# Optimization experiments

Hardware: AMD Instinct MI355X
Metric: run time of the kernel (lower is better)

Reference implementation:

```python
import jax, jax.numpy as jnp
import numpy as np

B, N, D, H = 32, 64, 64, 4
E = 4 * D
HD = E // H
EPS = 1e-10
TAU = 1.0


def _ln(x, g, b, eps=1e-5):
    m = x.mean(-1, keepdims=True)
    v = ((x - m) ** 2).mean(-1, keepdims=True)
    return (x - m) * jax.lax.rsqrt(v + eps) * g + b


def setup_inputs() -> dict:
    key = jax.random.key(0)
    ks = jax.random.split(key, 8)
    x = jax.random.normal(ks[0], (B, N, D), jnp.float32)
    A = jax.random.normal(ks[1], (B, N, N, 2 * D), jnp.float32)
    attn_mask = jax.random.randint(ks[2], (B, N, N), 0, 2).astype(jnp.int32)
    gumbel_u = jax.random.uniform(ks[3], (B, N, H, N), jnp.float32, minval=1e-6, maxval=1.0)
    in_proj_w = (jax.random.normal(ks[4], (3 * E, E), jnp.float32) * (E ** -0.5))
    in_proj_b = jnp.zeros((3 * E,), jnp.float32)
    w1 = jax.random.normal(ks[5], (HD, HD), jnp.float32) * (HD ** -0.5)
    b1 = jnp.zeros((HD,), jnp.float32)
    w2 = jax.random.normal(ks[6], (1, HD), jnp.float32) * (HD ** -0.5)
    b2 = jnp.zeros((1,), jnp.float32)
    return dict(x=x, A=A, attn_mask=attn_mask, gumbel_u=gumbel_u,
                ln_node_g=jnp.ones((D,), jnp.float32), ln_node_b=jnp.zeros((D,), jnp.float32),
                ln_edge_g=jnp.ones((2 * D,), jnp.float32), ln_edge_b=jnp.zeros((2 * D,), jnp.float32),
                in_proj_w=in_proj_w, in_proj_b=in_proj_b, w1=w1, b1=b1, w2=w2, b2=b2)


def reference(x, A, attn_mask, gumbel_u, ln_node_g, ln_node_b, ln_edge_g, ln_edge_b,
              in_proj_w, in_proj_b, w1, b1, w2, b2):
    b, n, d = x.shape
    e = 4 * d
    hd = e // H
    mask = attn_mask.astype(x.dtype)                      # (b, target, neighbor), 1/0
    ped = (mask.sum(-1) > 0).astype(x.dtype)[..., None]   # (b, n, 1)
    xn = _ln(x, ln_node_g, ln_node_b) * ped
    An = _ln(A, ln_edge_g, ln_edge_b) * jnp.transpose(mask, (0, 2, 1))[..., None]
    # broadcast concat: (b, neighbor, target, 4d)
    xneigh = jnp.broadcast_to(xn[:, :, None, :], (b, n, n, d))
    xtarg = jnp.broadcast_to(xn[:, None, :, :], (b, n, n, d))
    A4 = jnp.concatenate([xneigh, xtarg, An], axis=-1)
    Ap = jnp.transpose(A4, (0, 2, 1, 3))                  # (b, target, neighbor, 4d)
    # in-projection (torch MHA layout: rows [q; k; v])
    qkv = jnp.einsum('btme,fe->btmf', Ap, in_proj_w) + in_proj_b
    q, k, v = jnp.split(qkv, 3, axis=-1)
    q = q.reshape(b, n, n, H, hd) * (hd ** -0.5)
    k = k.reshape(b, n, n, H, hd)
    v = v.reshape(b, n, n, H, hd)
    scores = jnp.einsum('btjhd,btkhd->bthjk', q, k)       # per-target neighborhood attention
    m3 = mask[:, :, :, None] * mask[:, :, None, :]        # (b, t, j, k)
    w = jax.nn.softmax(scores, axis=-1) * m3[:, :, None, :, :]
    w = w / (w.sum(-1, keepdims=True) + EPS)
    A2 = jnp.einsum('bthjk,btkhd->bthjd', w, v)           # (b, target, head, neighbor, hd)
    hmid = jax.nn.relu(jnp.einsum('bthjd,od->bthjo', A2, w1) + b1)
    logits = (jnp.einsum('bthjo,xo->bthjx', hmid, w2) + b2)[..., 0]  # (b, t, h, j)
    em = jax.nn.softmax(logits, axis=-1) * mask[:, :, None, :]
    em = em / (em.sum(-1, keepdims=True) + EPS)
    g = -jnp.log(-jnp.log(gumbel_u + EPS) + EPS)
    sampled = jax.nn.softmax((jnp.log(em + EPS) + g) / TAU, axis=-1)
    return em, sampled
```

## Files before the change

kernel.cpp:

```cpp
#include <hip/hip_runtime.h>
#include <hip/hip_bf16.h>
#include <math.h>


typedef __attribute__((ext_vector_type(8))) short short8;
typedef __attribute__((ext_vector_type(4))) short short4v;
typedef __attribute__((ext_vector_type(4))) float f32x4;

__device__ __forceinline__ short f2b(float f) {
  return (short)__builtin_bit_cast(unsigned short, __float2bfloat16(f));
}

#define WCS 136
#define TS  72

#define OFF_K0  18432
#define OFF_VT0 36864
#define OFF_F   55296
#define LDS_BYTES 59904

__global__ __launch_bounds__(256) void k_node_ln(
    const float* __restrict__ x, const int* __restrict__ mask,
    const float* __restrict__ g, const float* __restrict__ bb,
    float* __restrict__ xn) {
  int tid = threadIdx.x;
  int row = blockIdx.x * 4 + (tid >> 6);
  int lane = tid & 63;
  float v = x[row * 64 + lane];
  float s = v;
#pragma unroll
  for (int m = 1; m < 64; m <<= 1) s += __shfl_xor(s, m, 64);
  float mean = s * (1.0f / 64.0f);
  float dv = v - mean;
  float s2 = dv * dv;
#pragma unroll
  for (int m = 1; m < 64; m <<= 1) s2 += __shfl_xor(s2, m, 64);
  float rstd = rsqrtf(s2 * (1.0f / 64.0f) + 1e-5f);
  float msum = (float)mask[row * 64 + lane];
#pragma unroll
  for (int m = 1; m < 64; m <<= 1) msum += __shfl_xor(msum, m, 64);
  float ped = (msum > 0.0f) ? 1.0f : 0.0f;
  xn[row * 64 + lane] = (dv * rstd * g[lane] + bb[lane]) * ped;
}

__global__ __launch_bounds__(256) void k_t12(
    const float* __restrict__ xn, const float* __restrict__ W,
    const float* __restrict__ bias, float* __restrict__ T1s, float* __restrict__ T2) {
  __shared__ __align__(16) float sx[8 * 64];
  int tid = threadIdx.x;
  int r0 = blockIdx.x * 8;
#pragma unroll
  for (int u = 0; u < 2; ++u) {
    int idx = tid + 256 * u;
    sx[idx] = xn[r0 * 64 + idx];
  }
  __syncthreads();
#pragma unroll
  for (int ff = 0; ff < 3; ++ff) {
    int f = tid + 256 * ff;
    float acc1[8], acc2[8];
#pragma unroll
    for (int r = 0; r < 8; ++r) { acc1[r] = 0.f; acc2[r] = 0.f; }
    for (int e4 = 0; e4 < 64; e4 += 4) {
      float4 wa = *(const float4*)&W[f * 256 + e4];
      float4 wb = *(const float4*)&W[f * 256 + 64 + e4];
#pragma unroll
      for (int r = 0; r < 8; ++r) {
        float4 xv = *(const float4*)&sx[r * 64 + e4];
        acc1[r] += wa.x * xv.x + wa.y * xv.y + wa.z * xv.z + wa.w * xv.w;
        acc2[r] += wb.x * xv.x + wb.y * xv.y + wb.z * xv.z + wb.w * xv.w;
      }
    }
    float bv = bias[f];
    int p = f >> 8, hh = (f >> 6) & 3, dcol = f & 63;
#pragma unroll
    for (int r = 0; r < 8; ++r) {
      int m = r0 + r;
      int bb2 = m >> 6, mm = m & 63;
      int wv_ = mm >> 4;
      int lane, reg;
      if (p < 2) {
        lane = ((dcol >> 2) & 3) * 16 + (mm & 15);
        reg = (dcol >> 4) * 4 + (dcol & 3);
      } else {
        lane = ((mm >> 2) & 3) * 16 + (dcol & 15);
        reg = (dcol >> 4) * 4 + (mm & 3);
      }
      T1s[(size_t)((((bb2 * 3 + p) * 4 + hh) * 4 + wv_) * 64 + lane) * 16 + reg] =
          acc1[r];
      T2[m * 768 + f] = acc2[r] + bv;
    }
  }
}

__global__ __launch_bounds__(256) void k_wb(const float* __restrict__ W,
                                            const float* __restrict__ w1,
                                            short* __restrict__ Wb,
                                            short* __restrict__ w1b) {
  int idx = blockIdx.x * 256 + threadIdx.x;
  if (idx < 12288) {
    int f = idx >> 4, gi = idx & 15;
    const float* src = &W[(size_t)f * 256 + 128 + gi * 8];
    short8 o;
#pragma unroll
    for (int i = 0; i < 8; ++i) o[i] = f2b(src[i]);
    *(short8*)&Wb[f * 128 + gi * 8] = o;
  } else if (idx < 12288 + 512) {
    int g2 = idx - 12288;
    int f = g2 >> 3, gi = g2 & 7;
    const float* src = &w1[f * 64 + gi * 8];
    short8 o;
#pragma unroll
    for (int i = 0; i < 8; ++i) o[i] = f2b(src[i]);
    *(short8*)&w1b[f * 64 + gi * 8] = o;
  }
}

__global__ __launch_bounds__(256, 2) void k_main(
    const float* __restrict__ A, const int* __restrict__ mask,
    const float* __restrict__ gu, const float* __restrict__ leg,
    const float* __restrict__ leb, const float* __restrict__ b1g,
    const float* __restrict__ w2g, const float* __restrict__ b2g,
    const float* __restrict__ T1s, const float* __restrict__ T2,
    const short* __restrict__ Wb, const short* __restrict__ w1b,
    float* __restrict__ out) {
  __shared__ __align__(16) unsigned char smem[LDS_BYTES];
  short* sWc = (short*)smem;
  float* sF  = (float*)(smem + OFF_F);

  int tid = threadIdx.x;
  int bid0 = blockIdx.x;
  int wg = (bid0 & 7) * 128 + (bid0 >> 3);
  int tq = wg & 31, b = wg >> 5;
  int t0 = tq * 2;
  int bt0 = b * 64 + t0;
  int wave = tid >> 6, lane = tid & 63, lr = lane & 15, lh = lane >> 4;

  if (tid < 64) sF[384 + tid] = (float)mask[bt0 * 64 + tid];
  else if (tid < 128) sF[448 + tid - 64] = (float)mask[(bt0 + 1) * 64 + tid - 64];
  else if (tid < 192) sF[512 + tid - 128] = b1g[tid - 128];
  else sF[576 + tid - 192] = w2g[tid - 192];

  short8 af[2][4];
  {
    int m0 = wave * 16 + lr;
    float4 a4[2][8];
    float mean[2], rstd[2], mv[2];
#pragma unroll
    for (int e = 0; e < 2; ++e) {
      const float* Ar = A + ((size_t)((b * 64 + m0) * 64 + t0 + e)) * 128;
#pragma unroll
      for (int ks = 0; ks < 4; ++ks) {
        a4[e][2 * ks]     = *(const float4*)&Ar[ks * 32 + lh * 8];
        a4[e][2 * ks + 1] = *(const float4*)&Ar[ks * 32 + lh * 8 + 4];
      }
      float s = 0.f, s2 = 0.f;
#pragma unroll
      for (int q = 0; q < 8; ++q) {
        float4 u0 = a4[e][q];
        s += u0.x + u0.y + u0.z + u0.w;
        s2 += u0.x * u0.x + u0.y * u0.y + u0.z * u0.z + u0.w * u0.w;
      }
      s += __shfl_xor(s, 16, 64);  s += __shfl_xor(s, 32, 64);
      s2 += __shfl_xor(s2, 16, 64); s2 += __shfl_xor(s2, 32, 64);
      mean[e] = s * (1.0f / 128.0f);
      float var = s2 * (1.0f / 128.0f) - mean[e] * mean[e];
      rstd[e] = rsqrtf(var + 1e-5f);
      mv[e] = (float)mask[(bt0 + e) * 64 + m0];
    }
#pragma unroll
    for (int ks = 0; ks < 4; ++ks) {
      float4 g0 = *(const float4*)&leg[ks * 32 + lh * 8];
      float4 g1 = *(const float4*)&leg[ks * 32 + lh * 8 + 4];
      float4 c0 = *(const float4*)&leb[ks * 32 + lh * 8];
      float4 c1 = *(const float4*)&leb[ks * 32 + lh * 8 + 4];
      float gg[8] = {g0.x, g0.y, g0.z, g0.w, g1.x, g1.y, g1.z, g1.w};
      float cc[8] = {c0.x, c0.y, c0.z, c0.w, c1.x, c1.y, c1.z, c1.w};
#pragma unroll
      for (int e = 0; e < 2; ++e) {
        float4 u0 = a4[e][2 * ks], u1 = a4[e][2 * ks + 1];
        float vv[8] = {u0.x, u0.y, u0.z, u0.w, u1.x, u1.y, u1.z, u1.w};
#pragma unroll
        for (int i = 0; i < 8; ++i)
          af[e][ks][i] = f2b(((vv[i] - mean[e]) * rstd[e] * gg[i] + cc[i]) * mv[e]);
      }
    }
  }

#pragma unroll 1
  for (int h = 0; h < 4; ++h) {
    __syncthreads();
    if (tid < 192) sF[tid] = T2[bt0 * 768 + (tid >> 6) * 256 + h * 64 + (tid & 63)];
    if (tid >= 64) {
      int i2 = tid - 64;
      sF[192 + i2] = T2[(bt0 + 1) * 768 + (i2 >> 6) * 256 + h * 64 + (i2 & 63)];
    }

#pragma unroll
    for (int pp = 0; pp < 3; ++pp) {
      const int p = (pp + 1) % 3;
      const int Fbase = p * 256 + h * 64;
#pragma unroll
      for (int u = 0; u < 4; ++u) {
        int idx = tid + 256 * u;
        int dR = idx >> 4, gi = idx & 15;
        *(short8*)&sWc[dR * WCS + gi * 8] =
            *(const short8*)&Wb[(size_t)(Fbase + dR) * 128 + gi * 8];
      }
      float4 t1f[4];
#pragma unroll
      for (int nt = 0; nt < 4; ++nt)
        t1f[nt] = *(const float4*)&T1s[
            (size_t)((((b * 3 + p) * 4 + h) * 4 + wave) * 64 + lane) * 16 + nt * 4];
      __syncthreads();
      f32x4 acc0[4], acc1[4];
#pragma unroll
      for (int nt = 0; nt < 4; ++nt) {
        acc0[nt][0] = t1f[nt].x; acc0[nt][1] = t1f[nt].y;
        acc0[nt][2] = t1f[nt].z; acc0[nt][3] = t1f[nt].w;
        acc1[nt] = acc0[nt];
      }
      if (p == 2) {
#pragma unroll
        for (int ks = 0; ks < 4; ++ks)
#pragma unroll
          for (int nt = 0; nt < 4; ++nt) {
            short8 bf = *(const short8*)&sWc[(nt * 16 + lr) * WCS + ks * 32 + lh * 8];
            acc0[nt] = __builtin_amdgcn_mfma_f32_16x16x32_bf16(af[0][ks], bf, acc0[nt], 0, 0, 0);
            acc1[nt] = __builtin_amdgcn_mfma_f32_16x16x32_bf16(af[1][ks], bf, acc1[nt], 0, 0, 0);
          }
      } else {
#pragma unroll
        for (int ks = 0; ks < 4; ++ks)
#pragma unroll
          for (int nt = 0; nt < 4; ++nt) {
            short8 bf = *(const short8*)&sWc[(nt * 16 + lr) * WCS + ks * 32 + lh * 8];
            acc0[nt] = __builtin_amdgcn_mfma_f32_16x16x32_bf16(bf, af[0][ks], acc0[nt], 0, 0, 0);
            acc1[nt] = __builtin_amdgcn_mfma_f32_16x16x32_bf16(bf, af[1][ks], acc1[nt], 0, 0, 0);
          }
      }
      if (p == 0) __syncthreads();
#pragma unroll
      for (int e = 0; e < 2; ++e) {
        const f32x4* acc = (e == 0) ? acc0 : acc1;
        if (p == 2) {
          short* sVTt = (short*)(smem + OFF_VT0 + e * 9216);
#pragma unroll
          for (int nt = 0; nt < 4; ++nt) {
            float t2v = sF[e * 192 + 128 + nt * 16 + lr];
            short4v vp;
#pragma unroll
            for (int r = 0; r < 4; ++r) vp[r] = f2b(acc[nt][r] + t2v);
            *(short4v*)&sVTt[(nt * 16 + lr) * TS + wave * 16 + lh * 4] = vp;
          }
        } else {
          float scale = (p == 0) ? 0.125f : 1.0f;
          short* dst = (p == 0) ? (short*)(smem + e * 9216)
                                : (short*)(smem + OFF_K0 + e * 9216);
#pragma unroll
          for (int nt = 0; nt < 4; ++nt) {
            float4 t24 = *(const float4*)&sF[e * 192 + p * 64 + nt * 16 + lh * 4];
            float tv[4] = {t24.x, t24.y, t24.z, t24.w};
            short4v qp;
#pragma unroll
            for (int r = 0; r < 4; ++r) qp[r] = f2b((acc[nt][r] + tv[r]) * scale);
            *(short4v*)&dst[(wave * 16 + lr) * TS + nt * 16 + lh * 4] = qp;
          }
        }
      }
      if (p != 0) __syncthreads();
    }

#pragma unroll
    for (int e = 0; e < 2; ++e) {
      short* sQt = (short*)(smem + e * 9216);
      short* sKt = (short*)(smem + OFF_K0 + e * 9216);
      f32x4 sc[4] = {};
#pragma unroll
      for (int ks = 0; ks < 2; ++ks) {
        short8 qf = *(const short8*)&sQt[(wave * 16 + lr) * TS + ks * 32 + lh * 8];
#pragma unroll
        for (int nt = 0; nt < 4; ++nt) {
          short8 kf = *(const short8*)&sKt[(nt * 16 + lr) * TS + ks * 32 + lh * 8];
          sc[nt] = __builtin_amdgcn_mfma_f32_16x16x32_bf16(kf, qf, sc[nt], 0, 0, 0);
        }
      }
      float mj = sF[384 + e * 64 + wave * 16 + lr];
      float mx = sc[0][0];
#pragma unroll
      for (int nt = 0; nt < 4; ++nt)
#pragma unroll
        for (int r = 0; r < 4; ++r) mx = fmaxf(mx, sc[nt][r]);
      mx = fmaxf(mx, __shfl_xor(mx, 16, 64));
      mx = fmaxf(mx, __shfl_xor(mx, 32, 64));
      float pv[4][4], mkv[4][4], Zf = 0.f, S = 0.f;
#pragma unroll
      for (int nt = 0; nt < 4; ++nt) {
        float4 mk4 = *(const float4*)&sF[384 + e * 64 + nt * 16 + lh * 4];
        float mk[4] = {mk4.x, mk4.y, mk4.z, mk4.w};
#pragma unroll
        for (int r = 0; r < 4; ++r) {
          float ev = __expf(sc[nt][r] - mx);
          pv[nt][r] = ev;
          mkv[nt][r] = mk[r];
          Zf += ev;
          S += ev * mk[r];
        }
      }
      Zf += __shfl_xor(Zf, 16, 64); Zf += __shfl_xor(Zf, 32, 64);
      S  += __shfl_xor(S, 16, 64);  S  += __shfl_xor(S, 32, 64);
      float inv = mj / (S + 1e-10f * Zf);
#pragma unroll
      for (int nt = 0; nt < 4; ++nt) {
        short4v wp;
#pragma unroll
        for (int r = 0; r < 4; ++r) wp[r] = f2b(pv[nt][r] * mkv[nt][r] * inv);
        *(short4v*)&sQt[(wave * 16 + lr) * TS + nt * 16 + lh * 4] = wp;
      }
    }
    __syncthreads();

#pragma unroll
    for (int e = 0; e < 2; ++e) {
      short* sWtt = (short*)(smem + e * 9216);
      short* sVTt = (short*)(smem + OFF_VT0 + e * 9216);
      short* sA2t = (short*)(smem + OFF_K0 + e * 9216);
      f32x4 a2[4] = {};
#pragma unroll
      for (int ks = 0; ks < 2; ++ks) {
        short8 wf = *(const short8*)&sWtt[(wave * 16 + lr) * TS + ks * 32 + lh * 8];
#pragma unroll
        for (int nt = 0; nt < 4; ++nt) {
          short8 vf = *(const short8*)&sVTt[(nt * 16 + lr) * TS + ks * 32 + lh * 8];
          a2[nt] = __builtin_amdgcn_mfma_f32_16x16x32_bf16(vf, wf, a2[nt], 0, 0, 0);
        }
      }
#pragma unroll
      for (int nt = 0; nt < 4; ++nt) {
        short4v ap;
#pragma unroll
        for (int r = 0; r < 4; ++r) ap[r] = f2b(a2[nt][r]);
        *(short4v*)&sA2t[(wave * 16 + lr) * TS + nt * 16 + lh * 4] = ap;
      }
      f32x4 hm[4] = {};
#pragma unroll
      for (int ks = 0; ks < 2; ++ks) {
        short8 a2f = *(const short8*)&sA2t[(wave * 16 + lr) * TS + ks * 32 + lh * 8];
#pragma unroll
        for (int nt = 0; nt < 4; ++nt) {
          short8 wf = *(const short8*)&w1b[(nt * 16 + lr) * 64 + ks * 32 + lh * 8];
          hm[nt] = __builtin_amdgcn_mfma_f32_16x16x32_bf16(wf, a2f, hm[nt], 0, 0, 0);
        }
      }
      float pp_ = 0.f;
#pragma unroll
      for (int nt = 0; nt < 4; ++nt) {
        float4 b14 = *(const float4*)&sF[512 + nt * 16 + lh * 4];
        float4 w24 = *(const float4*)&sF[576 + nt * 16 + lh * 4];
        float bb4[4] = {b14.x, b14.y, b14.z, b14.w};
        float ww4[4] = {w24.x, w24.y, w24.z, w24.w};
#pragma unroll
        for (int r = 0; r < 4; ++r)
          pp_ += fmaxf(hm[nt][r] + bb4[r], 0.f) * ww4[r];
      }
      pp_ += __shfl_xor(pp_, 16, 64);
      pp_ += __shfl_xor(pp_, 32, 64);
      if (lh == 0) sF[640 + (e * 4 + h) * 64 + wave * 16 + lr] = pp_;
    }
  }
  __syncthreads();

#pragma unroll
  for (int it = 0; it < 2; ++it) {
    int tile = it, hh = wave, j = lane;
    int btx = bt0 + tile;
    float l = sF[640 + (tile * 4 + hh) * 64 + j] + b2g[0];
    float mjv = sF[384 + tile * 64 + j];
    float mx = l;
#pragma unroll
    for (int mm = 1; mm < 64; mm <<= 1) mx = fmaxf(mx, __shfl_xor(mx, mm, 64));
    float pv = __expf(l - mx);
    float Z = pv;
#pragma unroll
    for (int mm = 1; mm < 64; mm <<= 1) Z += __shfl_xor(Z, mm, 64);
    float ep = (pv / Z) * mjv;
    float S = ep;
#pragma unroll
    for (int mm = 1; mm < 64; mm <<= 1) S += __shfl_xor(S, mm, 64);
    float em = ep / (S + 1e-10f);
    float u = gu[((size_t)btx * 4 + hh) * 64 + j];
    float gg = -__logf(-__logf(u + 1e-10f) + 1e-10f);
    float l2 = __logf(em + 1e-10f) + gg;
    float mx2 = l2;
#pragma unroll
    for (int mm = 1; mm < 64; mm <<= 1) mx2 = fmaxf(mx2, __shfl_xor(mx2, mm, 64));
    float p2 = __expf(l2 - mx2);
    float Z2 = p2;
#pragma unroll
    for (int mm = 1; mm < 64; mm <<= 1) Z2 += __shfl_xor(Z2, mm, 64);
    float smp = p2 / Z2;
    size_t o = ((size_t)btx * 4 + hh) * 64 + j;
    out[o] = em;
    out[524288 + o] = smp;
  }
}

extern "C" void kernel_launch(void* const* d_in, const int* in_sizes, int n_in,
                              void* d_out, int out_size, void* d_ws, size_t ws_size,
                              hipStream_t stream) {
  const float* x    = (const float*)d_in[0];
  const float* A    = (const float*)d_in[1];
  const int*   mask = (const int*)d_in[2];
  const float* gu   = (const float*)d_in[3];
  const float* lng  = (const float*)d_in[4];
  const float* lnb  = (const float*)d_in[5];
  const float* leg  = (const float*)d_in[6];
  const float* leb  = (const float*)d_in[7];
  const float* W    = (const float*)d_in[8];
  const float* bias = (const float*)d_in[9];
  const float* w1   = (const float*)d_in[10];
  const float* b1   = (const float*)d_in[11];
  const float* w2   = (const float*)d_in[12];
  const float* b2   = (const float*)d_in[13];
  float* out = (float*)d_out;
  float* ws  = (float*)d_ws;

  float* xn  = ws;
  float* T1s = xn + 131072;
  float* T2  = T1s + 1572864;
  short* Wb  = (short*)(T2 + 1572864);
  short* w1b = Wb + 98304;

  k_wb<<<50, 256, 0, stream>>>(W, w1, Wb, w1b);
  k_node_ln<<<512, 256, 0, stream>>>(x, mask, lng, lnb, xn);
  k_t12<<<256, 256, 0, stream>>>(xn, W, bias, T1s, T2);
  k_main<<<1024, 256, 0, stream>>>(A, mask, gu, leg, leb, b1, w2, b2,
                                   T1s, T2, Wb, w1b, out);
}
```

Baseline: 119.0 us.

## Keep Q, attention weights and A2 in registers via permuted MFMA layouts

Permutes the column order of the Q projection (including the T1s layout for p=0), the K rows and the w1 rows so that MFMA output fragments can be used directly as the next MFMA's input operands. This removes the LDS round trips for Q, softmax weights and A2, and lets K and V share one buffer, which shrinks LDS. The launch bound is raised to 4 blocks per CU, and LDS rows gain a small padding term to avoid bank conflicts. In exchange, register pressure rises under the tighter occupancy bound and the index permutations are intricate.

```diff
diff --git a/kernel.cpp b/kernel.cpp
--- a/kernel.cpp
+++ b/kernel.cpp
@@ -11,13 +11,13 @@
   return (short)__builtin_bit_cast(unsigned short, __float2bfloat16(f));
 }
 
-#define WCS 136
-#define TS  72
-
-#define OFF_K0  18432
-#define OFF_VT0 36864
-#define OFF_F   55296
-#define LDS_BYTES 59904
+#define ROW16(nt, i) ((((nt) >> 1) * 32) + (((i) >> 2) * 8) + (((nt) & 1) * 4) + ((i) & 3))
+__device__ __forceinline__ int phiA(int r) { return r * 136 + (r >> 3) * 8; }
+__device__ __forceinline__ int phiB(int r) { return r * 72 + (r >> 3) * 8; }
+
+#define OFF_B0 17504
+#define OFF_F  36128
+#define LDS_BYTES 40736
 
 __global__ __launch_bounds__(256) void k_node_ln(
     const float* __restrict__ x, const int* __restrict__ mask,
@@ -79,12 +79,15 @@
       int bb2 = m >> 6, mm = m & 63;
       int wv_ = mm >> 4;
       int lane, reg;
-      if (p < 2) {
+      if (p == 0) {
+        lane = ((dcol >> 3) & 3) * 16 + (mm & 15);
+        reg  = ((dcol >> 5) * 2 + ((dcol >> 2) & 1)) * 4 + (dcol & 3);
+      } else if (p == 1) {
         lane = ((dcol >> 2) & 3) * 16 + (mm & 15);
-        reg = (dcol >> 4) * 4 + (dcol & 3);
+        reg  = (dcol >> 4) * 4 + (dcol & 3);
       } else {
         lane = ((mm >> 2) & 3) * 16 + (dcol & 15);
-        reg = (dcol >> 4) * 4 + (mm & 3);
+        reg  = (dcol >> 4) * 4 + (mm & 3);
       }
       T1s[(size_t)((((bb2 * 3 + p) * 4 + hh) * 4 + wv_) * 64 + lane) * 16 + reg] =
           acc1[r];
@@ -116,7 +119,7 @@
   }
 }
 
-__global__ __launch_bounds__(256, 2) void k_main(
+__global__ __launch_bounds__(256, 4) void k_main(
     const float* __restrict__ A, const int* __restrict__ mask,
     const float* __restrict__ gu, const float* __restrict__ leg,
     const float* __restrict__ leb, const float* __restrict__ b1g,
@@ -135,6 +138,7 @@
   int t0 = tq * 2;
   int bt0 = b * 64 + t0;
   int wave = tid >> 6, lane = tid & 63, lr = lane & 15, lh = lane >> 4;
+  short* sB[2] = {(short*)(smem + OFF_B0), (short*)(smem + OFF_B0) + 4656};
 
   if (tid < 64) sF[384 + tid] = (float)mask[bt0 * 64 + tid];
   else if (tid < 128) sF[448 + tid - 64] = (float)mask[(bt0 + 1) * 64 + tid - 64];
@@ -187,6 +191,8 @@
     }
   }
 
+  short8 qf[2][2], wf[2][2];
+
 #pragma unroll 1
   for (int h = 0; h < 4; ++h) {
     __syncthreads();
@@ -195,24 +201,21 @@
       int i2 = tid - 64;
       sF[192 + i2] = T2[(bt0 + 1) * 768 + (i2 >> 6) * 256 + h * 64 + (i2 & 63)];
     }
-
-#pragma unroll
-    for (int pp = 0; pp < 3; ++pp) {
-      const int p = (pp + 1) % 3;
-      const int Fbase = p * 256 + h * 64;
-#pragma unroll
-      for (int u = 0; u < 4; ++u) {
-        int idx = tid + 256 * u;
-        int dR = idx >> 4, gi = idx & 15;
-        *(short8*)&sWc[dR * WCS + gi * 8] =
-            *(const short8*)&Wb[(size_t)(Fbase + dR) * 128 + gi * 8];
-      }
-      float4 t1f[4];
-#pragma unroll
-      for (int nt = 0; nt < 4; ++nt)
-        t1f[nt] = *(const float4*)&T1s[
-            (size_t)((((b * 3 + p) * 4 + h) * 4 + wave) * 64 + lane) * 16 + nt * 4];
-      __syncthreads();
+#pragma unroll
+    for (int u = 0; u < 4; ++u) {
+      int idx = tid + 256 * u;
+      int dR = idx >> 4, gi = idx & 15;
+      *(short8*)&sWc[phiA(dR) + gi * 8] =
+          *(const short8*)&Wb[(size_t)(h * 64 + dR) * 128 + gi * 8];
+    }
+    float4 t1f[4];
+#pragma unroll
+    for (int nt = 0; nt < 4; ++nt)
+      t1f[nt] = *(const float4*)&T1s[
+          (size_t)((((b * 3 + 0) * 4 + h) * 4 + wave) * 64 + lane) * 16 + nt * 4];
+    __syncthreads();
+
+    {
       f32x4 acc0[4], acc1[4];
 #pragma unroll
       for (int nt = 0; nt < 4; ++nt) {
@@ -220,71 +223,95 @@
         acc0[nt][2] = t1f[nt].z; acc0[nt][3] = t1f[nt].w;
         acc1[nt] = acc0[nt];
       }
-      if (p == 2) {
-#pragma unroll
-        for (int ks = 0; ks < 4; ++ks)
-#pragma unroll
-          for (int nt = 0; nt < 4; ++nt) {
-            short8 bf = *(const short8*)&sWc[(nt * 16 + lr) * WCS + ks * 32 + lh * 8];
-            acc0[nt] = __builtin_amdgcn_mfma_f32_16x16x32_bf16(af[0][ks], bf, acc0[nt], 0, 0, 0);
-            acc1[nt] = __builtin_amdgcn_mfma_f32_16x16x32_bf16(af[1][ks], bf, acc1[nt], 0, 0, 0);
-          }
-      } else {
-#pragma unroll
-        for (int ks = 0; ks < 4; ++ks)
-#pragma unroll
-          for (int nt = 0; nt < 4; ++nt) {
-            short8 bf = *(const short8*)&sWc[(nt * 16 + lr) * WCS + ks * 32 + lh * 8];
-            acc0[nt] = __builtin_amdgcn_mfma_f32_16x16x32_bf16(bf, af[0][ks], acc0[nt], 0, 0, 0);
-            acc1[nt] = __builtin_amdgcn_mfma_f32_16x16x32_bf16(bf, af[1][ks], acc1[nt], 0, 0, 0);
-          }
-      }
-      if (p == 0) __syncthreads();
+#pragma unroll
+      for (int ks = 0; ks < 4; ++ks)
+#pragma unroll
+        for (int nt = 0; nt < 4; ++nt) {
+          short8 bf = *(const short8*)&sWc[phiA(ROW16(nt, lr)) + ks * 32 + lh * 8];
+          acc0[nt] = __builtin_amdgcn_mfma_f32_16x16x32_bf16(bf, af[0][ks], acc0[nt], 0, 0, 0);
+          acc1[nt] = __builtin_amdgcn_mfma_f32_16x16x32_bf16(bf, af[1][ks], acc1[nt], 0, 0, 0);
+        }
 #pragma unroll
       for (int e = 0; e < 2; ++e) {
         const f32x4* acc = (e == 0) ? acc0 : acc1;
-        if (p == 2) {
-          short* sVTt = (short*)(smem + OFF_VT0 + e * 9216);
-#pragma unroll
-          for (int nt = 0; nt < 4; ++nt) {
-            float t2v = sF[e * 192 + 128 + nt * 16 + lr];
-            short4v vp;
-#pragma unroll
-            for (int r = 0; r < 4; ++r) vp[r] = f2b(acc[nt][r] + t2v);
-            *(short4v*)&sVTt[(nt * 16 + lr) * TS + wave * 16 + lh * 4] = vp;
-          }
-        } else {
-          float scale = (p == 0) ? 0.125f : 1.0f;
-          short* dst = (p == 0) ? (short*)(smem + e * 9216)
-                                : (short*)(smem + OFF_K0 + e * 9216);
-#pragma unroll
-          for (int nt = 0; nt < 4; ++nt) {
-            float4 t24 = *(const float4*)&sF[e * 192 + p * 64 + nt * 16 + lh * 4];
-            float tv[4] = {t24.x, t24.y, t24.z, t24.w};
-            short4v qp;
-#pragma unroll
-            for (int r = 0; r < 4; ++r) qp[r] = f2b((acc[nt][r] + tv[r]) * scale);
-            *(short4v*)&dst[(wave * 16 + lr) * TS + nt * 16 + lh * 4] = qp;
-          }
-        }
-      }
-      if (p != 0) __syncthreads();
-    }
+#pragma unroll
+        for (int nt = 0; nt < 4; ++nt) {
+          float4 t24 = *(const float4*)&sF[e * 192 + (nt >> 1) * 32 + (nt & 1) * 4 + lh * 8];
+          float tv[4] = {t24.x, t24.y, t24.z, t24.w};
+#pragma unroll
+          for (int r = 0; r < 4; ++r)
+            qf[e][nt >> 1][(nt & 1) * 4 + r] = f2b((acc[nt][r] + tv[r]) * 0.125f);
+        }
+      }
+    }
+    __syncthreads();
+#pragma unroll
+    for (int u = 0; u < 4; ++u) {
+      int idx = tid + 256 * u;
+      int dR = idx >> 4, gi = idx & 15;
+      *(short8*)&sWc[phiA(dR) + gi * 8] =
+          *(const short8*)&Wb[(size_t)(256 + h * 64 + dR) * 128 + gi * 8];
+    }
+#pragma unroll
+    for (int nt = 0; nt < 4; ++nt)
+      t1f[nt] = *(const float4*)&T1s[
+          (size_t)((((b * 3 + 1) * 4 + h) * 4 + wave) * 64 + lane) * 16 + nt * 4];
+    __syncthreads();
+
+    {
+      f32x4 acc0[4], acc1[4];
+#pragma unroll
+      for (int nt = 0; nt < 4; ++nt) {
+        acc0[nt][0] = t1f[nt].x; acc0[nt][1] = t1f[nt].y;
+        acc0[nt][2] = t1f[nt].z; acc0[nt][3] = t1f[nt].w;
+        acc1[nt] = acc0[nt];
+      }
+#pragma unroll
+      for (int ks = 0; ks < 4; ++ks)
+#pragma unroll
+        for (int nt = 0; nt < 4; ++nt) {
+          short8 bf = *(const short8*)&sWc[phiA(nt * 16 + lr) + ks * 32 + lh * 8];
+          acc0[nt] = __builtin_amdgcn_mfma_f32_16x16x32_bf16(bf, af[0][ks], acc0[nt], 0, 0, 0);
+          acc1[nt] = __builtin_amdgcn_mfma_f32_16x16x32_bf16(bf, af[1][ks], acc1[nt], 0, 0, 0);
+        }
+#pragma unroll
+      for (int e = 0; e < 2; ++e) {
+        const f32x4* acc = (e == 0) ? acc0 : acc1;
+#pragma unroll
+        for (int nt = 0; nt < 4; ++nt) {
+          float4 t24 = *(const float4*)&sF[e * 192 + 64 + nt * 16 + lh * 4];
+          float tv[4] = {t24.x, t24.y, t24.z, t24.w};
+          short4v kp;
+#pragma unroll
+          for (int r = 0; r < 4; ++r) kp[r] = f2b(acc[nt][r] + tv[r]);
+          *(short4v*)&sB[e][phiB(wave * 16 + lr) + nt * 16 + lh * 4] = kp;
+        }
+      }
+    }
+    __syncthreads();
+#pragma unroll
+    for (int u = 0; u < 4; ++u) {
+      int idx = tid + 256 * u;
+      int dR = idx >> 4, gi = idx & 15;
+      *(short8*)&sWc[phiA(dR) + gi * 8] =
+          *(const short8*)&Wb[(size_t)(512 + h * 64 + dR) * 128 + gi * 8];
+    }
+    float4 t1fv[4];
+#pragma unroll
+    for (int nt = 0; nt < 4; ++nt)
+      t1fv[nt] = *(const float4*)&T1s[
+          (size_t)((((b * 3 + 2) * 4 + h) * 4 + wave) * 64 + lane) * 16 + nt * 4];
 
 #pragma unroll
     for (int e = 0; e < 2; ++e) {
-      short* sQt = (short*)(smem + e * 9216);
-      short* sKt = (short*)(smem + OFF_K0 + e * 9216);
       f32x4 sc[4] = {};
 #pragma unroll
-      for (int ks = 0; ks < 2; ++ks) {
-        short8 qf = *(const short8*)&sQt[(wave * 16 + lr) * TS + ks * 32 + lh * 8];
-#pragma unroll
-        for (int nt = 0; nt < 4; ++nt) {
-          short8 kf = *(const short8*)&sKt[(nt * 16 + lr) * TS + ks * 32 + lh * 8];
-          sc[nt] = __builtin_amdgcn_mfma_f32_16x16x32_bf16(kf, qf, sc[nt], 0, 0, 0);
-        }
-      }
+      for (int ks = 0; ks < 2; ++ks)
+#pragma unroll
+        for (int nt = 0; nt < 4; ++nt) {
+          short8 kf = *(const short8*)&sB[e][phiB(ROW16(nt, lr)) + ks * 32 + lh * 8];
+          sc[nt] = __builtin_amdgcn_mfma_f32_16x16x32_bf16(kf, qf[e][ks], sc[nt], 0, 0, 0);
+        }
       float mj = sF[384 + e * 64 + wave * 16 + lr];
       float mx = sc[0][0];
 #pragma unroll
@@ -296,7 +323,7 @@
       float pv[4][4], mkv[4][4], Zf = 0.f, S = 0.f;
 #pragma unroll
       for (int nt = 0; nt < 4; ++nt) {
-        float4 mk4 = *(const float4*)&sF[384 + e * 64 + nt * 16 + lh * 4];
+        float4 mk4 = *(const float4*)&sF[384 + e * 64 + (nt >> 1) * 32 + (nt & 1) * 4 + lh * 8];
         float mk[4] = {mk4.x, mk4.y, mk4.z, mk4.w};
 #pragma unroll
         for (int r = 0; r < 4; ++r) {
@@ -311,52 +338,73 @@
       S  += __shfl_xor(S, 16, 64);  S  += __shfl_xor(S, 32, 64);
       float inv = mj / (S + 1e-10f * Zf);
 #pragma unroll
+      for (int nt = 0; nt < 4; ++nt)
+#pragma unroll
+        for (int r = 0; r < 4; ++r)
+          wf[e][nt >> 1][(nt & 1) * 4 + r] = f2b(pv[nt][r] * mkv[nt][r] * inv);
+    }
+    __syncthreads();
+
+    {
+      f32x4 acc0[4], acc1[4];
+#pragma unroll
       for (int nt = 0; nt < 4; ++nt) {
-        short4v wp;
-#pragma unroll
-        for (int r = 0; r < 4; ++r) wp[r] = f2b(pv[nt][r] * mkv[nt][r] * inv);
-        *(short4v*)&sQt[(wave * 16 + lr) * TS + nt * 16 + lh * 4] = wp;
+        acc0[nt][0] = t1fv[nt].x; acc0[nt][1] = t1fv[nt].y;
+        acc0[nt][2] = t1fv[nt].z; acc0[nt][3] = t1fv[nt].w;
+        acc1[nt] = acc0[nt];
+      }
+#pragma unroll
+      for (int ks = 0; ks < 4; ++ks)
+#pragma unroll
+        for (int nt = 0; nt < 4; ++nt) {
+          short8 bf = *(const short8*)&sWc[phiA(nt * 16 + lr) + ks * 32 + lh * 8];
+          acc0[nt] = __builtin_amdgcn_mfma_f32_16x16x32_bf16(af[0][ks], bf, acc0[nt], 0, 0, 0);
+          acc1[nt] = __builtin_amdgcn_mfma_f32_16x16x32_bf16(af[1][ks], bf, acc1[nt], 0, 0, 0);
+        }
+#pragma unroll
+      for (int e = 0; e < 2; ++e) {
+        const f32x4* acc = (e == 0) ? acc0 : acc1;
+#pragma unroll
+        for (int nt = 0; nt < 4; ++nt) {
+          float t2v = sF[e * 192 + 128 + nt * 16 + lr];
+          short4v vp;
+#pragma unroll
+          for (int r = 0; r < 4; ++r) vp[r] = f2b(acc[nt][r] + t2v);
+          *(short4v*)&sB[e][phiB(nt * 16 + lr) + wave * 16 + lh * 4] = vp;
+        }
       }
     }
     __syncthreads();
 
 #pragma unroll
     for (int e = 0; e < 2; ++e) {
-      short* sWtt = (short*)(smem + e * 9216);
-      short* sVTt = (short*)(smem + OFF_VT0 + e * 9216);
-      short* sA2t = (short*)(smem + OFF_K0 + e * 9216);
       f32x4 a2[4] = {};
 #pragma unroll
-      for (int ks = 0; ks < 2; ++ks) {
-        short8 wf = *(const short8*)&sWtt[(wave * 16 + lr) * TS + ks * 32 + lh * 8];
-#pragma unroll
-        for (int nt = 0; nt < 4; ++nt) {
-          short8 vf = *(const short8*)&sVTt[(nt * 16 + lr) * TS + ks * 32 + lh * 8];
-          a2[nt] = __builtin_amdgcn_mfma_f32_16x16x32_bf16(vf, wf, a2[nt], 0, 0, 0);
-        }
-      }
+      for (int ks = 0; ks < 2; ++ks)
+#pragma unroll
+        for (int nt = 0; nt < 4; ++nt) {
+          short8 vf = *(const short8*)&sB[e][phiB(ROW16(nt, lr)) + ks * 32 + lh * 8];
+          a2[nt] = __builtin_amdgcn_mfma_f32_16x16x32_bf16(vf, wf[e][ks], a2[nt], 0, 0, 0);
+        }
+      short8 a2f[2];
+#pragma unroll
+      for (int nt = 0; nt < 4; ++nt)
+#pragma unroll
+        for (int r = 0; r < 4; ++r)
+          a2f[nt >> 1][(nt & 1) * 4 + r] = f2b(a2[nt][r]);
+      f32x4 hm[4] = {};
+#pragma unroll
+      for (int ks = 0; ks < 2; ++ks)
+#pragma unroll
+        for (int nt = 0; nt < 4; ++nt) {
+          short8 w1f = *(const short8*)&w1b[ROW16(nt, lr) * 64 + ks * 32 + lh * 8];
+          hm[nt] = __builtin_amdgcn_mfma_f32_16x16x32_bf16(w1f, a2f[ks], hm[nt], 0, 0, 0);
+        }
+      float pp_ = 0.f;
 #pragma unroll
       for (int nt = 0; nt < 4; ++nt) {
-        short4v ap;
-#pragma unroll
-        for (int r = 0; r < 4; ++r) ap[r] = f2b(a2[nt][r]);
-        *(short4v*)&sA2t[(wave * 16 + lr) * TS + nt * 16 + lh * 4] = ap;
-      }
-      f32x4 hm[4] = {};
-#pragma unroll
-      for (int ks = 0; ks < 2; ++ks) {
-        short8 a2f = *(const short8*)&sA2t[(wave * 16 + lr) * TS + ks * 32 + lh * 8];
-#pragma unroll
-        for (int nt = 0; nt < 4; ++nt) {
-          short8 wf = *(const short8*)&w1b[(nt * 16 + lr) * 64 + ks * 32 + lh * 8];
-          hm[nt] = __builtin_amdgcn_mfma_f32_16x16x32_bf16(wf, a2f, hm[nt], 0, 0, 0);
-        }
-      }
-      float pp_ = 0.f;
-#pragma unroll
-      for (int nt = 0; nt < 4; ++nt) {
-        float4 b14 = *(const float4*)&sF[512 + nt * 16 + lh * 4];
-        float4 w24 = *(const float4*)&sF[576 + nt * 16 + lh * 4];
+        float4 b14 = *(const float4*)&sF[512 + (nt >> 1) * 32 + (nt & 1) * 4 + lh * 8];
+        float4 w24 = *(const float4*)&sF[576 + (nt >> 1) * 32 + (nt & 1) * 4 + lh * 8];
         float bb4[4] = {b14.x, b14.y, b14.z, b14.w};
         float ww4[4] = {w24.x, w24.y, w24.z, w24.w};
 #pragma unroll
```

Result: slower. 146.9 us (+23.5%).

## Software-pipeline weight and T1/T2 loads across projection phases via registers

Applied to the files above, without the earlier changes.

Unrolls the three per-head projection phases (K, V, Q) and prefetches the next phase's bf16 weight tile, T1 slice and T2 bias into registers while the current phase runs its MFMAs. Each staged tile is then written to LDS at the start of the next phase, which hides the global load latency that used to sit directly before a barrier. It also precomputes load offsets and drops the launch-bounds occupancy hint of two blocks per CU. That gives the compiler room for the extra prefetch registers, at the risk of lower occupancy.

```diff
diff --git a/kernel.cpp b/kernel.cpp
--- a/kernel.cpp
+++ b/kernel.cpp
@@ -81,10 +81,10 @@
       int lane, reg;
       if (p < 2) {
         lane = ((dcol >> 2) & 3) * 16 + (mm & 15);
-        reg = (dcol >> 4) * 4 + (dcol & 3);
+        reg  = (dcol >> 4) * 4 + (dcol & 3);
       } else {
         lane = ((mm >> 2) & 3) * 16 + (dcol & 15);
-        reg = (dcol >> 4) * 4 + (mm & 3);
+        reg  = (dcol >> 4) * 4 + (mm & 3);
       }
       T1s[(size_t)((((bb2 * 3 + p) * 4 + hh) * 4 + wv_) * 64 + lane) * 16 + reg] =
           acc1[r];
@@ -116,7 +116,7 @@
   }
 }
 
-__global__ __launch_bounds__(256, 2) void k_main(
+__global__ __launch_bounds__(256) void k_main(
     const float* __restrict__ A, const int* __restrict__ mask,
     const float* __restrict__ gu, const float* __restrict__ leg,
     const float* __restrict__ leb, const float* __restrict__ b1g,
@@ -136,6 +136,17 @@
   int bt0 = b * 64 + t0;
   int wave = tid >> 6, lane = tid & 63, lr = lane & 15, lh = lane >> 4;
 
+  int wb_off[4], lds_off[4];
+#pragma unroll
+  for (int u = 0; u < 4; ++u) {
+    int idx = tid + 256 * u, dR = idx >> 4, gi = idx & 15;
+    wb_off[u]  = dR * 128 + gi * 8;
+    lds_off[u] = dR * WCS + gi * 8;
+  }
+  int t2i0 = (tid >> 6) * 256 + (tid & 63);
+  int i2 = tid - 64;
+  int t2i1 = (i2 >> 6) * 256 + (i2 & 63);
+
   if (tid < 64) sF[384 + tid] = (float)mask[bt0 * 64 + tid];
   else if (tid < 128) sF[448 + tid - 64] = (float)mask[(bt0 + 1) * 64 + tid - 64];
   else if (tid < 192) sF[512 + tid - 128] = b1g[tid - 128];
@@ -187,88 +198,162 @@
     }
   }
 
+  short8 wcreg[4];
+  float4 t1n[4];
+  float t2r0 = 0.f, t2r1 = 0.f;
+#pragma unroll
+  for (int u = 0; u < 4; ++u)
+    wcreg[u] = *(const short8*)&Wb[(size_t)256 * 128 + wb_off[u]];
+#pragma unroll
+  for (int nt = 0; nt < 4; ++nt)
+    t1n[nt] = *(const float4*)&T1s[
+        (size_t)((((b * 3 + 1) * 4 + 0) * 4 + wave) * 64 + lane) * 16 + nt * 4];
+  if (tid < 192) t2r0 = T2[bt0 * 768 + t2i0];
+  if (tid >= 64) t2r1 = T2[(bt0 + 1) * 768 + t2i1];
+
 #pragma unroll 1
   for (int h = 0; h < 4; ++h) {
     __syncthreads();
-    if (tid < 192) sF[tid] = T2[bt0 * 768 + (tid >> 6) * 256 + h * 64 + (tid & 63)];
-    if (tid >= 64) {
-      int i2 = tid - 64;
-      sF[192 + i2] = T2[(bt0 + 1) * 768 + (i2 >> 6) * 256 + h * 64 + (i2 & 63)];
-    }
-
-#pragma unroll
-    for (int pp = 0; pp < 3; ++pp) {
-      const int p = (pp + 1) % 3;
-      const int Fbase = p * 256 + h * 64;
-#pragma unroll
-      for (int u = 0; u < 4; ++u) {
-        int idx = tid + 256 * u;
-        int dR = idx >> 4, gi = idx & 15;
-        *(short8*)&sWc[dR * WCS + gi * 8] =
-            *(const short8*)&Wb[(size_t)(Fbase + dR) * 128 + gi * 8];
-      }
-      float4 t1f[4];
-#pragma unroll
-      for (int nt = 0; nt < 4; ++nt)
-        t1f[nt] = *(const float4*)&T1s[
-            (size_t)((((b * 3 + p) * 4 + h) * 4 + wave) * 64 + lane) * 16 + nt * 4];
-      __syncthreads();
+#pragma unroll
+    for (int u = 0; u < 4; ++u) *(short8*)&sWc[lds_off[u]] = wcreg[u];
+    if (tid < 192) sF[tid] = t2r0;
+    if (tid >= 64) sF[192 + i2] = t2r1;
+    float4 t1c[4];
+#pragma unroll
+    for (int nt = 0; nt < 4; ++nt) t1c[nt] = t1n[nt];
+#pragma unroll
+    for (int u = 0; u < 4; ++u)
+      wcreg[u] = *(const short8*)&Wb[(size_t)(512 + h * 64) * 128 + wb_off[u]];
+#pragma unroll
+    for (int nt = 0; nt < 4; ++nt)
+      t1n[nt] = *(const float4*)&T1s[
+          (size_t)((((b * 3 + 2) * 4 + h) * 4 + wave) * 64 + lane) * 16 + nt * 4];
+    __syncthreads();
+
+    {
       f32x4 acc0[4], acc1[4];
 #pragma unroll
       for (int nt = 0; nt < 4; ++nt) {
-        acc0[nt][0] = t1f[nt].x; acc0[nt][1] = t1f[nt].y;
-        acc0[nt][2] = t1f[nt].z; acc0[nt][3] = t1f[nt].w;
+        acc0[nt][0] = t1c[nt].x; acc0[nt][1] = t1c[nt].y;
+        acc0[nt][2] = t1c[nt].z; acc0[nt][3] = t1c[nt].w;
         acc1[nt] = acc0[nt];
       }
-      if (p == 2) {
-#pragma unroll
-        for (int ks = 0; ks < 4; ++ks)
-#pragma unroll
-          for (int nt = 0; nt < 4; ++nt) {
-            short8 bf = *(const short8*)&sWc[(nt * 16 + lr) * WCS + ks * 32 + lh * 8];
-            acc0[nt] = __builtin_amdgcn_mfma_f32_16x16x32_bf16(af[0][ks], bf, acc0[nt], 0, 0, 0);
-            acc1[nt] = __builtin_amdgcn_mfma_f32_16x16x32_bf16(af[1][ks], bf, acc1[nt], 0, 0, 0);
-          }
-      } else {
-#pragma unroll
-        for (int ks = 0; ks < 4; ++ks)
-#pragma unroll
-          for (int nt = 0; nt < 4; ++nt) {
-            short8 bf = *(const short8*)&sWc[(nt * 16 + lr) * WCS + ks * 32 + lh * 8];
-            acc0[nt] = __builtin_amdgcn_mfma_f32_16x16x32_bf16(bf, af[0][ks], acc0[nt], 0, 0, 0);
-            acc1[nt] = __builtin_amdgcn_mfma_f32_16x16x32_bf16(bf, af[1][ks], acc1[nt], 0, 0, 0);
-          }
-      }
-      if (p == 0) __syncthreads();
+#pragma unroll
+      for (int ks = 0; ks < 4; ++ks)
+#pragma unroll
+        for (int nt = 0; nt < 4; ++nt) {
+          short8 bf = *(const short8*)&sWc[(nt * 16 + lr) * WCS + ks * 32 + lh * 8];
+          acc0[nt] = __builtin_amdgcn_mfma_f32_16x16x32_bf16(bf, af[0][ks], acc0[nt], 0, 0, 0);
+          acc1[nt] = __builtin_amdgcn_mfma_f32_16x16x32_bf16(bf, af[1][ks], acc1[nt], 0, 0, 0);
+        }
 #pragma unroll
       for (int e = 0; e < 2; ++e) {
         const f32x4* acc = (e == 0) ? acc0 : acc1;
-        if (p == 2) {
-          short* sVTt = (short*)(smem + OFF_VT0 + e * 9216);
-#pragma unroll
-          for (int nt = 0; nt < 4; ++nt) {
-            float t2v = sF[e * 192 + 128 + nt * 16 + lr];
-            short4v vp;
-#pragma unroll
-            for (int r = 0; r < 4; ++r) vp[r] = f2b(acc[nt][r] + t2v);
-            *(short4v*)&sVTt[(nt * 16 + lr) * TS + wave * 16 + lh * 4] = vp;
-          }
-        } else {
-          float scale = (p == 0) ? 0.125f : 1.0f;
-          short* dst = (p == 0) ? (short*)(smem + e * 9216)
-                                : (short*)(smem + OFF_K0 + e * 9216);
-#pragma unroll
-          for (int nt = 0; nt < 4; ++nt) {
-            float4 t24 = *(const float4*)&sF[e * 192 + p * 64 + nt * 16 + lh * 4];
-            float tv[4] = {t24.x, t24.y, t24.z, t24.w};
-            short4v qp;
-#pragma unroll
-            for (int r = 0; r < 4; ++r) qp[r] = f2b((acc[nt][r] + tv[r]) * scale);
-            *(short4v*)&dst[(wave * 16 + lr) * TS + nt * 16 + lh * 4] = qp;
-          }
-        }
-      }
-      if (p != 0) __syncthreads();
+        short* sKt = (short*)(smem + OFF_K0 + e * 9216);
+#pragma unroll
+        for (int nt = 0; nt < 4; ++nt) {
+          float4 t24 = *(const float4*)&sF[e * 192 + 64 + nt * 16 + lh * 4];
+          float tv[4] = {t24.x, t24.y, t24.z, t24.w};
+          short4v kp;
+#pragma unroll
+          for (int r = 0; r < 4; ++r) kp[r] = f2b(acc[nt][r] + tv[r]);
+          *(short4v*)&sKt[(wave * 16 + lr) * TS + nt * 16 + lh * 4] = kp;
+        }
+      }
+    }
+    __syncthreads();
+#pragma unroll
+    for (int u = 0; u < 4; ++u) *(short8*)&sWc[lds_off[u]] = wcreg[u];
+#pragma unroll
+    for (int nt = 0; nt < 4; ++nt) t1c[nt] = t1n[nt];
+#pragma unroll
+    for (int u = 0; u < 4; ++u)
+      wcreg[u] = *(const short8*)&Wb[(size_t)(h * 64) * 128 + wb_off[u]];
+#pragma unroll
+    for (int nt = 0; nt < 4; ++nt)
+      t1n[nt] = *(const float4*)&T1s[
+          (size_t)((((b * 3 + 0) * 4 + h) * 4 + wave) * 64 + lane) * 16 + nt * 4];
+    __syncthreads();
+
+    {
+      f32x4 acc0[4], acc1[4];
+#pragma unroll
+      for (int nt = 0; nt < 4; ++nt) {
+        acc0[nt][0] = t1c[nt].x; acc0[nt][1] = t1c[nt].y;
+        acc0[nt][2] = t1c[nt].z; acc0[nt][3] = t1c[nt].w;
+        acc1[nt] = acc0[nt];
+      }
+#pragma unroll
+      for (int ks = 0; ks < 4; ++ks)
+#pragma unroll
+        for (int nt = 0; nt < 4; ++nt) {
+          short8 bf = *(const short8*)&sWc[(nt * 16 + lr) * WCS + ks * 32 + lh * 8];
+          acc0[nt] = __builtin_amdgcn_mfma_f32_16x16x32_bf16(af[0][ks], bf, acc0[nt], 0, 0, 0);
+          acc1[nt] = __builtin_amdgcn_mfma_f32_16x16x32_bf16(af[1][ks], bf, acc1[nt], 0, 0, 0);
+        }
+#pragma unroll
+      for (int e = 0; e < 2; ++e) {
+        const f32x4* acc = (e == 0) ? acc0 : acc1;
+        short* sVTt = (short*)(smem + OFF_VT0 + e * 9216);
+#pragma unroll
+        for (int nt = 0; nt < 4; ++nt) {
+          float t2v = sF[e * 192 + 128 + nt * 16 + lr];
+          short4v vp;
+#pragma unroll
+          for (int r = 0; r < 4; ++r) vp[r] = f2b(acc[nt][r] + t2v);
+          *(short4v*)&sVTt[(nt * 16 + lr) * TS + wave * 16 + lh * 4] = vp;
+        }
+      }
+    }
+    __syncthreads();
+#pragma unroll
+    for (int u = 0; u < 4; ++u) *(short8*)&sWc[lds_off[u]] = wcreg[u];
+#pragma unroll
+    for (int nt = 0; nt < 4; ++nt) t1c[nt] = t1n[nt];
+    if (h < 3) {
+#pragma unroll
+      for (int u = 0; u < 4; ++u)
+        wcreg[u] = *(const short8*)&Wb[(size_t)(256 + (h + 1) * 64) * 128 + wb_off[u]];
+#pragma unroll
+      for (int nt = 0; nt < 4; ++nt)
+        t1n[nt] = *(const float4*)&T1s[
+            (size_t)((((b * 3 + 1) * 4 + (h + 1)) * 4 + wave) * 64 + lane) * 16 + nt * 4];
+      if (tid < 192) t2r0 = T2[bt0 * 768 + (h + 1) * 64 + t2i0];
+      if (tid >= 64) t2r1 = T2[(bt0 + 1) * 768 + (h + 1) * 64 + t2i1];
+    }
+    __syncthreads();
+
+    f32x4 qacc0[4], qacc1[4];
+    {
+#pragma unroll
+      for (int nt = 0; nt < 4; ++nt) {
+        qacc0[nt][0] = t1c[nt].x; qacc0[nt][1] = t1c[nt].y;
+        qacc0[nt][2] = t1c[nt].z; qacc0[nt][3] = t1c[nt].w;
+        qacc1[nt] = qacc0[nt];
+      }
+#pragma unroll
+      for (int ks = 0; ks < 4; ++ks)
+#pragma unroll
+        for (int nt = 0; nt < 4; ++nt) {
+          short8 bf = *(const short8*)&sWc[(nt * 16 + lr) * WCS + ks * 32 + lh * 8];
+          qacc0[nt] = __builtin_amdgcn_mfma_f32_16x16x32_bf16(bf, af[0][ks], qacc0[nt], 0, 0, 0);
+          qacc1[nt] = __builtin_amdgcn_mfma_f32_16x16x32_bf16(bf, af[1][ks], qacc1[nt], 0, 0, 0);
+        }
+    }
+    __syncthreads();
+#pragma unroll
+    for (int e = 0; e < 2; ++e) {
+      const f32x4* acc = (e == 0) ? qacc0 : qacc1;
+      short* sQt = (short*)(smem + e * 9216);
+#pragma unroll
+      for (int nt = 0; nt < 4; ++nt) {
+        float4 t24 = *(const float4*)&sF[e * 192 + nt * 16 + lh * 4];
+        float tv[4] = {t24.x, t24.y, t24.z, t24.w};
+        short4v qp;
+#pragma unroll
+        for (int r = 0; r < 4; ++r) qp[r] = f2b((acc[nt][r] + tv[r]) * 0.125f);
+        *(short4v*)&sQt[(wave * 16 + lr) * TS + nt * 16 + lh * 4] = qp;
+      }
     }
 
 #pragma unroll
@@ -278,11 +363,11 @@
       f32x4 sc[4] = {};
 #pragma unroll
       for (int ks = 0; ks < 2; ++ks) {
-        short8 qf = *(const short8*)&sQt[(wave * 16 + lr) * TS + ks * 32 + lh * 8];
+        short8 qfr = *(const short8*)&sQt[(wave * 16 + lr) * TS + ks * 32 + lh * 8];
 #pragma unroll
         for (int nt = 0; nt < 4; ++nt) {
           short8 kf = *(const short8*)&sKt[(nt * 16 + lr) * TS + ks * 32 + lh * 8];
-          sc[nt] = __builtin_amdgcn_mfma_f32_16x16x32_bf16(kf, qf, sc[nt], 0, 0, 0);
+          sc[nt] = __builtin_amdgcn_mfma_f32_16x16x32_bf16(kf, qfr, sc[nt], 0, 0, 0);
         }
       }
       float mj = sF[384 + e * 64 + wave * 16 + lr];
@@ -328,11 +413,11 @@
       f32x4 a2[4] = {};
 #pragma unroll
       for (int ks = 0; ks < 2; ++ks) {
-        short8 wf = *(const short8*)&sWtt[(wave * 16 + lr) * TS + ks * 32 + lh * 8];
+        short8 wfr = *(const short8*)&sWtt[(wave * 16 + lr) * TS + ks * 32 + lh * 8];
 #pragma unroll
         for (int nt = 0; nt < 4; ++nt) {
           short8 vf = *(const short8*)&sVTt[(nt * 16 + lr) * TS + ks * 32 + lh * 8];
-          a2[nt] = __builtin_amdgcn_mfma_f32_16x16x32_bf16(vf, wf, a2[nt], 0, 0, 0);
+          a2[nt] = __builtin_amdgcn_mfma_f32_16x16x32_bf16(vf, wfr, a2[nt], 0, 0, 0);
         }
       }
 #pragma unroll
@@ -348,8 +433,8 @@
         short8 a2f = *(const short8*)&sA2t[(wave * 16 + lr) * TS + ks * 32 + lh * 8];
 #pragma unroll
         for (int nt = 0; nt < 4; ++nt) {
-          short8 wf = *(const short8*)&w1b[(nt * 16 + lr) * 64 + ks * 32 + lh * 8];
-          hm[nt] = __builtin_amdgcn_mfma_f32_16x16x32_bf16(wf, a2f, hm[nt], 0, 0, 0);
+          short8 wf1 = *(const short8*)&w1b[(nt * 16 + lr) * 64 + ks * 32 + lh * 8];
+          hm[nt] = __builtin_amdgcn_mfma_f32_16x16x32_bf16(wf1, a2f, hm[nt], 0, 0, 0);
         }
       }
       float pp_ = 0.f;
```

After: 155.8 us. 30.9% more time.
